# Performance work log

Hardware: AMD Instinct MI355X
Metric: run time of the kernel (lower is better)

Reference implementation:

```python
import jax, jax.numpy as jnp
import numpy as np

TAU = 2.0   # spikingjelly LIFNode default tau
VTH = 1.0   # config.vthreshold

@jax.custom_vjp
def atan_spike(x):
    # heaviside forward, ATan surrogate backward (spikingjelly surrogate.ATan, alpha=2)
    return (x >= 0).astype(x.dtype)

def _atan_fwd(x):
    return atan_spike(x), x

def _atan_bwd(x, g):
    alpha = 2.0
    return (g * (alpha / 2.0) / (1.0 + (jnp.pi / 2.0 * alpha * x) ** 2),)

atan_spike.defvjp(_atan_fwd, _atan_bwd)

def layer_norm(x, eps=1e-6):
    m = jnp.mean(x, axis=-1, keepdims=True)
    v = jnp.mean((x - m) ** 2, axis=-1, keepdims=True)
    return (x - m) * jax.lax.rsqrt(v + eps)

def time_shift(x):
    # ZeroPad2d((0,0,1,-1)): xx[:, t] = x[:, t-1], xx[:, 0] = 0
    return jnp.pad(x, ((0, 0), (1, 0), (0, 0)))[:, :-1]

def lif_multistep(x4):
    # spikingjelly LIFNode, step_mode='m', decay_input=True, hard reset to v_reset=0
    def step(v, xt):
        v = v + (xt - v) / TAU
        s = atan_spike(v - VTH)
        return v * (1.0 - s), s
    _, spikes = jax.lax.scan(step, jnp.zeros_like(x4[0]), x4)
    return spikes

def wkv(w, u, k, v):
    # RWKV-v4 numerically-stable WKV scan. w: [C] (negative), u: [C], k,v: [B,T,C]
    B, T, C = k.shape
    def step(carry, kv):
        aa, bb, pp = carry
        kt, vt = kv
        ww = u + kt
        p = jnp.maximum(pp, ww)
        e1 = jnp.exp(pp - p); e2 = jnp.exp(ww - p)
        y = (e1 * aa + e2 * vt) / (e1 * bb + e2)
        ww2 = pp + w
        p2 = jnp.maximum(ww2, kt)
        f1 = jnp.exp(ww2 - p2); f2 = jnp.exp(kt - p2)
        return (f1 * aa + f2 * vt, f1 * bb + f2, p2), y
    init = (jnp.zeros((B, C), k.dtype), jnp.zeros((B, C), k.dtype),
            jnp.full((B, C), -1e38, k.dtype))
    _, ys = jax.lax.scan(step, init, (jnp.moveaxis(k, 1, 0), jnp.moveaxis(v, 1, 0)))
    return jnp.moveaxis(ys, 0, 1)

def time_mix(h, time_decay, time_first, tmk, tmv, tmr, Wk, Wv, Wr, Wo):
    xx = time_shift(h)
    xk = h * tmk + xx * (1 - tmk)
    xv = h * tmv + xx * (1 - tmv)
    xr = h * tmr + xx * (1 - tmr)
    k = jnp.einsum('btc,oc->bto', xk, Wk)
    v = jnp.einsum('btc,oc->bto', xv, Wv)
    sr = jax.nn.sigmoid(jnp.einsum('btc,oc->bto', xr, Wr))
    y = wkv(-jnp.exp(time_decay), time_first, k, v)
    return jnp.einsum('btc,oc->bto', sr * y, Wo)

def channel_mix(h, cmk, cmr, Wck, Wcv, Wcr):
    xx = time_shift(h)
    xk = h * cmk + xx * (1 - cmk)
    xr = h * cmr + xx * (1 - cmr)
    k = jnp.square(jax.nn.relu(jnp.einsum('btc,hc->bth', xk, Wck)))
    kv = jnp.einsum('bth,ch->btc', k, Wcv)
    return jax.nn.sigmoid(jnp.einsum('btc,oc->bto', xr, Wcr)) * kv

def _forward(x, rt, time_decay, time_first, tmix_k, tmix_v, tmix_r,
             Wk, Wv, Wr, Wo, cmix_k, cmix_r, Wck, Wcv, Wcr,
             Wrm, brm, Wam, bam):
    B, P1, C = x.shape
    xc = jnp.concatenate([x, jnp.broadcast_to(rt, (B, P1, C))], axis=1)  # [B, 2*P1, C]
    att = time_mix(layer_norm(xc), time_decay, time_first,
                   tmix_k, tmix_v, tmix_r, Wk, Wv, Wr, Wo)
    att = lif_multistep(jnp.broadcast_to(att, (4,) + att.shape)).mean(0)
    xc = xc + att
    ffn = channel_mix(layer_norm(xc), cmix_k, cmix_r, Wck, Wcv, Wcr)
    ffn = lif_multistep(jnp.broadcast_to(ffn, (4,) + ffn.shape)).mean(0)
    xc = xc + ffn
    xo, rtok = xc[:, :P1], xc[:, P1:]
    r = jnp.einsum('bpc,qc->bpq', rtok, Wrm) + brm   # restruction_token_MLP [B,P1,P1]
    r = jnp.swapaxes(r, 1, 2)                        # permute(0,2,1)
    r = jnp.einsum('bpq,cq->bpc', r, Wam) + bam      # another_MLP [B,P1,C]
    return xo + xo * r

def setup_inputs() -> dict:
    key = jax.random.key(0)
    ks = jax.random.split(key, 20)
    B, P1, C = 8, 256, 1024
    H = 4 * C
    s = 0.02
    f32 = jnp.float32
    return {
        'x': jax.random.normal(ks[0], (B, P1, C), f32),
        'rt': jax.random.normal(ks[1], (1, P1, C), f32) * 0.5,
        'time_decay': jax.random.normal(ks[2], (C,), f32),
        'time_first': jax.random.normal(ks[3], (C,), f32) * 0.3,
        'tmix_k': jax.random.uniform(ks[4], (1, 1, C), f32),
        'tmix_v': jax.random.uniform(ks[5], (1, 1, C), f32),
        'tmix_r': jax.random.uniform(ks[6], (1, 1, C), f32),
        'Wk': jax.random.normal(ks[7], (C, C), f32) * s,
        'Wv': jax.random.normal(ks[8], (C, C), f32) * s,
        'Wr': jax.random.normal(ks[9], (C, C), f32) * s,
        'Wo': jax.random.normal(ks[10], (C, C), f32) * s,
        'cmix_k': jax.random.uniform(ks[11], (1, 1, C), f32),
        'cmix_r': jax.random.uniform(ks[12], (1, 1, C), f32),
        'Wck': jax.random.normal(ks[13], (H, C), f32) * s,
        'Wcv': jax.random.normal(ks[14], (C, H), f32) * s,
        'Wcr': jax.random.normal(ks[15], (C, C), f32) * s,
        'Wrm': jax.random.normal(ks[16], (P1, C), f32) * s,
        'brm': jax.random.normal(ks[17], (P1,), f32) * s,
        'Wam': jax.random.normal(ks[18], (C, P1), f32) * s,
        'bam': jax.random.normal(ks[19], (C,), f32) * s,
    }

def reference(x, rt, time_decay, time_first, tmix_k, tmix_v, tmix_r,
              Wk, Wv, Wr, Wo, cmix_k, cmix_r, Wck, Wcv, Wcr,
              Wrm, brm, Wam, bam):
    return _forward(x, rt, time_decay, time_first, tmix_k, tmix_v, tmix_r,
                    Wk, Wv, Wr, Wo, cmix_k, cmix_r, Wck, Wcv, Wcr,
                    Wrm, brm, Wam, bam)
```

## Files before the change

kernel.cpp:

```cpp
#include <hip/hip_runtime.h>
#include <hip/hip_bf16.h>
#include <math.h>
#include <stdint.h>

#define TB_ 8
#define TT_ 512
#define TC_ 1024
#define WKV_NCH 32
#define WKV_L 16

typedef __attribute__((ext_vector_type(8))) short bf16x8;
typedef __attribute__((ext_vector_type(4))) short s16x4;
typedef __attribute__((ext_vector_type(4))) float f32x4;

__device__ __forceinline__ float b2f(short u) {
  union { unsigned int i; float f; } x;
  x.i = ((unsigned int)(unsigned short)u) << 16;
  return x.f;
}
__device__ __forceinline__ short f2b(float f) {
  __hip_bfloat16 h = __float2bfloat16(f);
  return __builtin_bit_cast(short, h);
}
__device__ __forceinline__ float sigm(float x) { return 1.0f / (1.0f + expf(-x)); }

__device__ __forceinline__ float lif4(float a) {
  float v = 0.0f, acc = 0.0f;
#pragma unroll
  for (int i = 0; i < 4; ++i) {
    v += (a - v) * 0.5f;
    float s = (v >= 1.0f) ? 1.0f : 0.0f;
    acc += s;
    v *= (1.0f - s);
  }
  return acc * 0.25f;
}

__device__ __forceinline__ void gload16(const void* g, void* l) {
  __builtin_amdgcn_global_load_lds(
      (__attribute__((address_space(1))) void*)(g),
      (__attribute__((address_space(3))) void*)(l), 16, 0, 0);
}

template <int N>
__device__ __forceinline__ void waitv() {
  if constexpr (N == 0)  asm volatile("s_waitcnt vmcnt(0)" ::: "memory");
  else if constexpr (N == 2)  asm volatile("s_waitcnt vmcnt(2)" ::: "memory");
  else if constexpr (N == 3)  asm volatile("s_waitcnt vmcnt(3)" ::: "memory");
  else if constexpr (N == 4)  asm volatile("s_waitcnt vmcnt(4)" ::: "memory");
  else if constexpr (N == 6)  asm volatile("s_waitcnt vmcnt(6)" ::: "memory");
  else if constexpr (N == 8)  asm volatile("s_waitcnt vmcnt(8)" ::: "memory");
  else if constexpr (N == 9)  asm volatile("s_waitcnt vmcnt(9)" ::: "memory");
  else if constexpr (N == 12) asm volatile("s_waitcnt vmcnt(12)" ::: "memory");
  else static_assert(N == 0, "unsupported vmcnt");
}
__device__ __forceinline__ void barrier_() {
  asm volatile("s_barrier" ::: "memory");
}


__global__ __launch_bounds__(256) void build_xc(const float* __restrict__ x,
                                                const float* __restrict__ rt,
                                                float* __restrict__ xc) {
  int i = blockIdx.x * 256 + threadIdx.x;
  int c4 = i & 255;
  int t = (i >> 8) & 511;
  int b = i >> 17;
  float4 v;
  if (t < 256)
    v = ((const float4*)x)[(b * 256 + t) * 256 + c4];
  else
    v = ((const float4*)rt)[(t - 256) * 256 + c4];
  ((float4*)xc)[i] = v;
}

__global__ __launch_bounds__(256) void ln_rows_b(const float* __restrict__ src,
                                                 short* __restrict__ dst) {
  __shared__ float red[256];
  int64_t row = blockIdx.x;
  float4 v = ((const float4*)(src + row * TC_))[threadIdx.x];
  red[threadIdx.x] = v.x + v.y + v.z + v.w;
  __syncthreads();
  for (int off = 128; off > 0; off >>= 1) {
    if (threadIdx.x < off) red[threadIdx.x] += red[threadIdx.x + off];
    __syncthreads();
  }
  float mean = red[0] * (1.0f / 1024.0f);
  __syncthreads();
  float dx = v.x - mean, dy = v.y - mean, dz = v.z - mean, dw = v.w - mean;
  red[threadIdx.x] = dx * dx + dy * dy + dz * dz + dw * dw;
  __syncthreads();
  for (int off = 128; off > 0; off >>= 1) {
    if (threadIdx.x < off) red[threadIdx.x] += red[threadIdx.x + off];
    __syncthreads();
  }
  float rs = 1.0f / sqrtf(red[0] * (1.0f / 1024.0f) + 1e-6f);
  s16x4 o;
  o.x = f2b(dx * rs); o.y = f2b(dy * rs); o.z = f2b(dz * rs); o.w = f2b(dw * rs);
  *(s16x4*)(dst + row * TC_ + threadIdx.x * 4) = o;
}

__global__ __launch_bounds__(256) void mix3_b(const short* __restrict__ ln,
                                              const float* __restrict__ tk,
                                              const float* __restrict__ tv,
                                              const float* __restrict__ tr,
                                              short* __restrict__ xk,
                                              short* __restrict__ xv,
                                              short* __restrict__ xr) {
  int i = blockIdx.x * 256 + threadIdx.x;
  int c8 = i & 127;
  int t = (i >> 7) & 511;
  bf16x8 h = *(const bf16x8*)(ln + (int64_t)i * 8);
  bf16x8 s = {};
  if (t > 0) s = *(const bf16x8*)(ln + (int64_t)(i - 128) * 8);
  bf16x8 ok, ov, orr;
#pragma unroll
  for (int e = 0; e < 8; ++e) {
    float hf = b2f(h[e]), sf = b2f(s[e]);
    int c = c8 * 8 + e;
    float mk = tk[c], mv = tv[c], mr = tr[c];
    ok[e] = f2b(hf * mk + sf * (1.0f - mk));
    ov[e] = f2b(hf * mv + sf * (1.0f - mv));
    orr[e] = f2b(hf * mr + sf * (1.0f - mr));
  }
  *(bf16x8*)(xk + (int64_t)i * 8) = ok;
  *(bf16x8*)(xv + (int64_t)i * 8) = ov;
  *(bf16x8*)(xr + (int64_t)i * 8) = orr;
}

__global__ __launch_bounds__(256) void mix2_b(const short* __restrict__ ln,
                                              const float* __restrict__ tk,
                                              const float* __restrict__ tr,
                                              short* __restrict__ xk,
                                              short* __restrict__ xr) {
  int i = blockIdx.x * 256 + threadIdx.x;
  int c8 = i & 127;
  int t = (i >> 7) & 511;
  bf16x8 h = *(const bf16x8*)(ln + (int64_t)i * 8);
  bf16x8 s = {};
  if (t > 0) s = *(const bf16x8*)(ln + (int64_t)(i - 128) * 8);
  bf16x8 ok, orr;
#pragma unroll
  for (int e = 0; e < 8; ++e) {
    float hf = b2f(h[e]), sf = b2f(s[e]);
    int c = c8 * 8 + e;
    float mk = tk[c], mr = tr[c];
    ok[e] = f2b(hf * mk + sf * (1.0f - mk));
    orr[e] = f2b(hf * mr + sf * (1.0f - mr));
  }
  *(bf16x8*)(xk + (int64_t)i * 8) = ok;
  *(bf16x8*)(xr + (int64_t)i * 8) = orr;
}

__global__ __launch_bounds__(256) void cvt_b(const float* __restrict__ src,
                                             short* __restrict__ dst) {
  int64_t i = (int64_t)(blockIdx.x * 256 + threadIdx.x) * 8;
  float4 a = *(const float4*)(src + i);
  float4 b = *(const float4*)(src + i + 4);
  bf16x8 o;
  o[0] = f2b(a.x); o[1] = f2b(a.y); o[2] = f2b(a.z); o[3] = f2b(a.w);
  o[4] = f2b(b.x); o[5] = f2b(b.y); o[6] = f2b(b.z); o[7] = f2b(b.w);
  *(bf16x8*)(dst + i) = o;
}

__global__ __launch_bounds__(256) void cvt_rtok(const float* __restrict__ xc,
                                                short* __restrict__ dst) {
  int i = blockIdx.x * 256 + threadIdx.x;
  int b = i >> 15;
  int rem = i & 32767;
  const float* s = xc + (int64_t)b * 524288 + 262144 + (int64_t)rem * 8;
  float4 a = *(const float4*)s;
  float4 c = *(const float4*)(s + 4);
  bf16x8 o;
  o[0] = f2b(a.x); o[1] = f2b(a.y); o[2] = f2b(a.z); o[3] = f2b(a.w);
  o[4] = f2b(c.x); o[5] = f2b(c.y); o[6] = f2b(c.z); o[7] = f2b(c.w);
  *(bf16x8*)(dst + (int64_t)i * 8) = o;
}

__global__ __launch_bounds__(256) void wkv_p1(const float* __restrict__ td,
                                              const short* __restrict__ K,
                                              const short* __restrict__ V,
                                              float* __restrict__ Ca,
                                              float* __restrict__ Da,
                                              float* __restrict__ Qa) {
  int bx = blockIdx.x;
  int ch = bx >> 5;
  int b = (bx >> 2) & 7;
  int c = (bx & 3) * 256 + threadIdx.x;
  float w = -expf(td[c]);
  float aa = 0.0f, bb = 0.0f, pp = -1e38f;
  int64_t base = ((int64_t)b * TT_ + ch * WKV_L) * TC_ + c;
#pragma unroll
  for (int t = 0; t < WKV_L; ++t) {
    int64_t o = base + (int64_t)t * TC_;
    float kt = b2f(K[o]), vt = b2f(V[o]);
    float ww2 = pp + w;
    float p2 = fmaxf(ww2, kt);
    float e1 = expf(ww2 - p2);
    float e2 = expf(kt - p2);
    aa = e1 * aa + e2 * vt;
    bb = e1 * bb + e2;
    pp = p2;
  }
  int idx = ch * 8192 + b * 1024 + c;
  Ca[idx] = aa; Da[idx] = bb; Qa[idx] = pp;
}

__global__ __launch_bounds__(256) void wkv_p2(const float* __restrict__ td,
                                              const float* __restrict__ Ca,
                                              const float* __restrict__ Da,
                                              const float* __restrict__ Qa,
                                              float* __restrict__ Aa,
                                              float* __restrict__ Ba,
                                              float* __restrict__ Pa) {
  int i = blockIdx.x * 256 + threadIdx.x;
  int c = i & (TC_ - 1);
  float wL = -expf(td[c]) * (float)WKV_L;
  float aa = 0.0f, bb = 0.0f, pp = -1e38f;
#pragma unroll 4
  for (int ch = 0; ch < WKV_NCH; ++ch) {
    int idx = ch * 8192 + i;
    Aa[idx] = aa; Ba[idx] = bb; Pa[idx] = pp;
    float ppw = pp + wL;
    float q = Qa[idx];
    float p2 = fmaxf(ppw, q);
    float ea = expf(ppw - p2);
    float eb = expf(q - p2);
    aa = aa * ea + Ca[idx] * eb;
    bb = bb * ea + Da[idx] * eb;
    pp = p2;
  }
}

__global__ __launch_bounds__(256) void wkv_p3(const float* __restrict__ td,
                                              const float* __restrict__ tf,
                                              const short* __restrict__ K,
                                              const short* __restrict__ V,
                                              const short* __restrict__ SR,
                                              short* __restrict__ SRY,
                                              const float* __restrict__ Aa,
                                              const float* __restrict__ Ba,
                                              const float* __restrict__ Pa) {
  int bx = blockIdx.x;
  int ch = bx >> 5;
  int b = (bx >> 2) & 7;
  int c = (bx & 3) * 256 + threadIdx.x;
  float w = -expf(td[c]);
  float u = tf[c];
  int idx = ch * 8192 + b * 1024 + c;
  float aa = Aa[idx], bb = Ba[idx], pp = Pa[idx];
  int64_t base = ((int64_t)b * TT_ + ch * WKV_L) * TC_ + c;
#pragma unroll
  for (int t = 0; t < WKV_L; ++t) {
    int64_t o = base + (int64_t)t * TC_;
    float kt = b2f(K[o]), vt = b2f(V[o]);
    float ww = u + kt;
    float p = fmaxf(pp, ww);
    float E1 = expf(pp - p);
    float E2 = expf(ww - p);
    float y = (E1 * aa + E2 * vt) / (E1 * bb + E2);
    SRY[o] = f2b(y * b2f(SR[o]));
    float ww2 = pp + w;
    float p2 = fmaxf(ww2, kt);
    float e1 = expf(ww2 - p2);
    float e2 = expf(kt - p2);
    aa = e1 * aa + e2 * vt;
    bb = e1 * bb + e2;
    pp = p2;
  }
}

__global__ __launch_bounds__(64) void row_sum256(const float* __restrict__ Wam,
                                                 float* __restrict__ S) {
  int c = blockIdx.x;
  int lane = threadIdx.x;
  float4 v = ((const float4*)(Wam + (int64_t)c * 256))[lane];
  float s = v.x + v.y + v.z + v.w;
  for (int off = 32; off > 0; off >>= 1) s += __shfl_down(s, off);
  if (lane == 0) S[c] = s;
}

template <int BM, int BN, int EPI>
__global__ __launch_bounds__(256, 2) void gemm_bf16(
    const short* __restrict__ A, const short* __restrict__ B,
    void* __restrict__ Cp, int M, int N, int K,
    int64_t sA, int64_t sB, int64_t sC,
    const float* __restrict__ e0, const float* __restrict__ e1,
    const float* __restrict__ e2, const void* __restrict__ e3, int64_t sE) {
  constexpr int MF = BM / 32;
  constexpr int NF = BN / 32;
  constexpr int ASLOT = BM / 64;
  constexpr int BSLOT = BN / 64;
  constexpr int NL = ASLOT + BSLOT;
  constexpr int SBUF = (BM + BN) * 32;
  constexpr int D = 4;
  __shared__ short lds[D * SBUF];
  const int tid = threadIdx.x;

  const unsigned gx = gridDim.x, gy = gridDim.y;
  const unsigned nwg = gx * gy * gridDim.z;
  const unsigned lin = blockIdx.x + gx * (blockIdx.y + gy * blockIdx.z);
  const unsigned cs = nwg >> 3;
  const unsigned nl = (lin & 7) * cs + (lin >> 3);
  const unsigned bxs = nl % gx;
  const unsigned tmp = nl / gx;
  const unsigned bys = tmp % gy;
  const unsigned bz = tmp / gy;

  const int brow = bys * BM;
  const int bcol = bxs * BN;
  const short* Ab = A + bz * sA;
  const short* Bb = B + bz * sB;

  const int srow = ((tid >> 6) << 4) + (tid & 15);
  const int skc = ((tid >> 4) & 3) * 8;
  const short* gA[ASLOT];
  const short* gB[BSLOT];
#pragma unroll
  for (int s = 0; s < ASLOT; ++s)
    gA[s] = Ab + (int64_t)(brow + s * 64 + srow) * K + skc;
#pragma unroll
  for (int s = 0; s < BSLOT; ++s)
    gB[s] = Bb + (int64_t)(bcol + s * 64 + srow) * K + skc;

  const int lane = tid & 63, wid = tid >> 6;
  const int wr = wid >> 1, wc = wid & 1;

  f32x4 acc[MF][NF] = {};

  auto stage = [&](int buf, int k0) {
    short* d = lds + buf * SBUF;
#pragma unroll
    for (int s = 0; s < ASLOT; ++s)
      gload16(gA[s] + k0, d + s * 2048 + tid * 8);
#pragma unroll
    for (int s = 0; s < BSLOT; ++s)
      gload16(gB[s] + k0, d + BM * 32 + s * 2048 + tid * 8);
  };
  auto compute = [&](int buf) {
    const short* base = lds + buf * SBUF;
    bf16x8 af[MF], bfv[NF];
#pragma unroll
    for (int m = 0; m < MF; ++m)
      af[m] = *(const bf16x8*)(base + (wr * MF + m) * 512 + lane * 8);
#pragma unroll
    for (int n = 0; n < NF; ++n)
      bfv[n] = *(const bf16x8*)(base + BM * 32 + (wc * NF + n) * 512 + lane * 8);
#pragma unroll
    for (int m = 0; m < MF; ++m)
#pragma unroll
      for (int n = 0; n < NF; ++n)
        acc[m][n] = __builtin_amdgcn_mfma_f32_16x16x32_bf16(af[m], bfv[n],
                                                            acc[m][n], 0, 0, 0);
  };

  const int nst = K / 32;
#pragma unroll
  for (int d = 0; d < D - 1; ++d) stage(d, d * 32);
  for (int t = 0; t <= nst - D; ++t) {
    stage((t + D - 1) & (D - 1), (t + D - 1) * 32);
    waitv<(D - 1) * NL>();
    barrier_();
    compute(t & (D - 1));
    barrier_();
  }
  {
    int t = nst - D + 1;
    waitv<2 * NL>(); barrier_(); compute(t & (D - 1)); barrier_(); ++t;
    waitv<1 * NL>(); barrier_(); compute(t & (D - 1)); barrier_(); ++t;
    waitv<0>();      barrier_(); compute(t & (D - 1));
  }

  const int r0 = brow + wr * (BM / 2) + (lane >> 4) * 4;
  const int c0 = bcol + wc * (BN / 2) + (lane & 15);
#pragma unroll
  for (int m = 0; m < MF; ++m) {
#pragma unroll
    for (int j = 0; j < 4; ++j) {
      int row = r0 + m * 16 + j;
#pragma unroll
      for (int n = 0; n < NF; ++n) {
        int col = c0 + n * 16;
        float v = acc[m][n][j];
        int64_t idx = (int64_t)row * N + col;
        if (EPI == 0) {
          ((short*)Cp)[bz * sC + idx] = f2b(v);
        } else if (EPI == 1) {
          ((short*)Cp)[bz * sC + idx] = f2b(sigm(v));
        } else if (EPI == 2) {
          v = fmaxf(v, 0.0f);
          ((short*)Cp)[bz * sC + idx] = f2b(v * v);
        } else if (EPI == 3) {
          float r2 = v + e0[row] * e1[col] + e2[col];
          float xo = ((const float*)e3)[bz * sE + idx];
          ((float*)Cp)[bz * sC + idx] = xo * (1.0f + r2);
        } else if (EPI == 4) {
          float* XC = (float*)Cp;
          XC[idx] = XC[idx] + lif4(v);
        } else if (EPI == 5) {
          float* XC = (float*)Cp;
          float srr = b2f(((const short*)e3)[idx]);
          XC[idx] = XC[idx] + lif4(v * srr);
        } else if (EPI == 6) {
          ((short*)Cp)[bz * sC + idx] = f2b(bz == 2 ? sigm(v) : v);
        }
      }
    }
  }
}

extern "C" void kernel_launch(void* const* d_in, const int* in_sizes, int n_in,
                              void* d_out, int out_size, void* d_ws,
                              size_t ws_size, hipStream_t stream) {
  const float* x   = (const float*)d_in[0];
  const float* rt  = (const float*)d_in[1];
  const float* td  = (const float*)d_in[2];
  const float* tf  = (const float*)d_in[3];
  const float* tmk = (const float*)d_in[4];
  const float* tmv = (const float*)d_in[5];
  const float* tmr = (const float*)d_in[6];
  const float* Wk  = (const float*)d_in[7];
  const float* Wv  = (const float*)d_in[8];
  const float* Wr  = (const float*)d_in[9];
  const float* Wo  = (const float*)d_in[10];
  const float* cmk = (const float*)d_in[11];
  const float* cmr = (const float*)d_in[12];
  const float* Wck = (const float*)d_in[13];
  const float* Wcv = (const float*)d_in[14];
  const float* Wcr = (const float*)d_in[15];
  const float* Wrm = (const float*)d_in[16];
  const float* brm = (const float*)d_in[17];
  const float* Wam = (const float*)d_in[18];
  const float* bam = (const float*)d_in[19];
  float* out = (float*)d_out;

  const size_t MB = 1ull << 20;
  uint8_t* W8 = (uint8_t*)d_ws;
  float* XC   = (float*)(W8);
  short* L    = (short*)(W8 + 16 * MB);
  short* S1   = (short*)(W8 + 24 * MB);
  short* S2   = (short*)(W8 + 32 * MB);
  short* S3   = (short*)(W8 + 40 * MB);
  short* bWcv = (short*)(W8 + 48 * MB);
  short* bWk  = (short*)(W8 + 56 * MB);
  short* bWo  = (short*)(W8 + 62 * MB);
  short* bWcr = (short*)(W8 + 64 * MB);
  short* bWrm = (short*)(W8 + 66 * MB);
  short* bWam = (short*)(W8 + 66 * MB + 512 * 1024);
  short* KK   = (short*)(W8 + 67 * MB);
  short* VV   = (short*)(W8 + 75 * MB);
  short* RR   = (short*)(W8 + 83 * MB);
  float* Ca   = (float*)(W8 + 91 * MB);
  float* Da   = (float*)(W8 + 92 * MB);
  float* Qa   = (float*)(W8 + 93 * MB);
  float* Aa   = (float*)(W8 + 94 * MB);
  float* Ba   = (float*)(W8 + 95 * MB);
  float* Pa   = (float*)(W8 + 96 * MB);
  short* SRY  = S1;
  short* xk2  = S2;
  short* xr2  = S3;
  short* SRR  = S1;
  short* bWck = S3;
  short* H16  = KK;
  short* rtok = S2;
  short* Mt   = (short*)(W8 + 36 * MB);
  float* Sb   = (float*)(W8 + 24 * MB);

  dim3 blk(256);
  const int NV4 = 4096;
  const int NV8 = 2048;

  cvt_b<<<512, blk, 0, stream>>>(Wk, bWk);
  cvt_b<<<512, blk, 0, stream>>>(Wv, bWk + 1048576);
  cvt_b<<<512, blk, 0, stream>>>(Wr, bWk + 2097152);
  cvt_b<<<512, blk, 0, stream>>>(Wo, bWo);
  cvt_b<<<512, blk, 0, stream>>>(Wcr, bWcr);
  cvt_b<<<128, blk, 0, stream>>>(Wrm, bWrm);
  cvt_b<<<128, blk, 0, stream>>>(Wam, bWam);

  build_xc<<<NV4, blk, 0, stream>>>(x, rt, XC);
  ln_rows_b<<<TB_ * TT_, blk, 0, stream>>>(XC, L);
  mix3_b<<<NV8, blk, 0, stream>>>(L, tmk, tmv, tmr, S1, S2, S3);

  gemm_bf16<128, 128, 6><<<dim3(8, 32, 3), blk, 0, stream>>>(
      S1, bWk, KK, 4096, 1024, 1024, 4194304, 1048576, 4194304,
      nullptr, nullptr, nullptr, nullptr, 0);
  wkv_p1<<<WKV_NCH * TB_ * 4, blk, 0, stream>>>(td, KK, VV, Ca, Da, Qa);
  wkv_p2<<<32, blk, 0, stream>>>(td, Ca, Da, Qa, Aa, Ba, Pa);
  wkv_p3<<<WKV_NCH * TB_ * 4, blk, 0, stream>>>(td, tf, KK, VV, RR, SRY,
                                                Aa, Ba, Pa);
  gemm_bf16<128, 128, 4><<<dim3(8, 32, 1), blk, 0, stream>>>(
      SRY, bWo, XC, 4096, 1024, 1024, 0, 0, 0,
      nullptr, nullptr, nullptr, nullptr, 0);
  ln_rows_b<<<TB_ * TT_, blk, 0, stream>>>(XC, L);
  mix2_b<<<NV8, blk, 0, stream>>>(L, cmk, cmr, xk2, xr2);
  gemm_bf16<128, 128, 1><<<dim3(8, 32, 1), blk, 0, stream>>>(
      xr2, bWcr, SRR, 4096, 1024, 1024, 0, 0, 0,
      nullptr, nullptr, nullptr, nullptr, 0);
  cvt_b<<<2048, blk, 0, stream>>>(Wck, bWck);
  cvt_b<<<2048, blk, 0, stream>>>(Wcv, bWcv);
  gemm_bf16<128, 128, 2><<<dim3(32, 32, 1), blk, 0, stream>>>(
      xk2, bWck, H16, 4096, 4096, 1024, 0, 0, 0,
      nullptr, nullptr, nullptr, nullptr, 0);
  gemm_bf16<128, 128, 5><<<dim3(8, 32, 1), blk, 0, stream>>>(
      H16, bWcv, XC, 4096, 1024, 4096, 0, 0, 0,
      nullptr, nullptr, nullptr, SRR, 0);
  cvt_rtok<<<1024, blk, 0, stream>>>(XC, rtok);
  gemm_bf16<64, 64, 0><<<dim3(4, 4, 8), blk, 0, stream>>>(
      bWrm, rtok, Mt, 256, 256, 1024, 0, (int64_t)256 * 1024,
      (int64_t)256 * 256, nullptr, nullptr, nullptr, nullptr, 0);
  row_sum256<<<1024, dim3(64), 0, stream>>>(Wam, Sb);
  gemm_bf16<64, 64, 3><<<dim3(16, 4, 8), blk, 0, stream>>>(
      Mt, bWam, out, 256, 1024, 256, (int64_t)256 * 256, 0,
      (int64_t)256 * 1024, brm, Sb, bam, XC, (int64_t)512 * 1024);
}
```

Before: 355.8 us.

## Tune GEMM pipeline depth and occupancy per call; fuse input gather with LayerNorm

The GEMM kernel now takes its LDS pipeline depth and minimum-waves launch bound as template parameters, with matching vmcnt waits and tail handling for depths 2, 4 and 8. Each call site picks its own setting: deep 8-stage pipelines at one wave-group per CU for the K-heavy or small-grid GEMMs, and shallow 2-stage pipelines with higher occupancy for the others. Separately, the copy kernel that concatenated x and rt is fused into the first LayerNorm, so the assembled rows are read once and written alongside the normalized output. The risks are larger LDS use (128KB at depth 8) lowering occupancy, and less latency hiding at depth 2.

```diff
diff --git a/kernel.cpp b/kernel.cpp
--- a/kernel.cpp
+++ b/kernel.cpp
@@ -46,12 +46,14 @@
 __device__ __forceinline__ void waitv() {
   if constexpr (N == 0)  asm volatile("s_waitcnt vmcnt(0)" ::: "memory");
   else if constexpr (N == 2)  asm volatile("s_waitcnt vmcnt(2)" ::: "memory");
-  else if constexpr (N == 3)  asm volatile("s_waitcnt vmcnt(3)" ::: "memory");
   else if constexpr (N == 4)  asm volatile("s_waitcnt vmcnt(4)" ::: "memory");
   else if constexpr (N == 6)  asm volatile("s_waitcnt vmcnt(6)" ::: "memory");
   else if constexpr (N == 8)  asm volatile("s_waitcnt vmcnt(8)" ::: "memory");
-  else if constexpr (N == 9)  asm volatile("s_waitcnt vmcnt(9)" ::: "memory");
   else if constexpr (N == 12) asm volatile("s_waitcnt vmcnt(12)" ::: "memory");
+  else if constexpr (N == 16) asm volatile("s_waitcnt vmcnt(16)" ::: "memory");
+  else if constexpr (N == 20) asm volatile("s_waitcnt vmcnt(20)" ::: "memory");
+  else if constexpr (N == 24) asm volatile("s_waitcnt vmcnt(24)" ::: "memory");
+  else if constexpr (N == 28) asm volatile("s_waitcnt vmcnt(28)" ::: "memory");
   else static_assert(N == 0, "unsupported vmcnt");
 }
 __device__ __forceinline__ void barrier_() {
@@ -59,19 +61,36 @@
 }
 
 
-__global__ __launch_bounds__(256) void build_xc(const float* __restrict__ x,
+__global__ __launch_bounds__(256) void ln_first(const float* __restrict__ x,
                                                 const float* __restrict__ rt,
-                                                float* __restrict__ xc) {
-  int i = blockIdx.x * 256 + threadIdx.x;
-  int c4 = i & 255;
-  int t = (i >> 8) & 511;
-  int b = i >> 17;
-  float4 v;
-  if (t < 256)
-    v = ((const float4*)x)[(b * 256 + t) * 256 + c4];
-  else
-    v = ((const float4*)rt)[(t - 256) * 256 + c4];
-  ((float4*)xc)[i] = v;
+                                                float* __restrict__ xc,
+                                                short* __restrict__ dst) {
+  __shared__ float red[256];
+  int row = blockIdx.x;
+  int t = row & 511, b = row >> 9;
+  const float* src = (t < 256) ? x + (int64_t)(b * 256 + t) * TC_
+                               : rt + (int64_t)(t - 256) * TC_;
+  float4 v = ((const float4*)src)[threadIdx.x];
+  ((float4*)(xc + (int64_t)row * TC_))[threadIdx.x] = v;
+  red[threadIdx.x] = v.x + v.y + v.z + v.w;
+  __syncthreads();
+  for (int off = 128; off > 0; off >>= 1) {
+    if (threadIdx.x < off) red[threadIdx.x] += red[threadIdx.x + off];
+    __syncthreads();
+  }
+  float mean = red[0] * (1.0f / 1024.0f);
+  __syncthreads();
+  float dx = v.x - mean, dy = v.y - mean, dz = v.z - mean, dw = v.w - mean;
+  red[threadIdx.x] = dx * dx + dy * dy + dz * dz + dw * dw;
+  __syncthreads();
+  for (int off = 128; off > 0; off >>= 1) {
+    if (threadIdx.x < off) red[threadIdx.x] += red[threadIdx.x + off];
+    __syncthreads();
+  }
+  float rs = 1.0f / sqrtf(red[0] * (1.0f / 1024.0f) + 1e-6f);
+  s16x4 o;
+  o.x = f2b(dx * rs); o.y = f2b(dy * rs); o.z = f2b(dz * rs); o.w = f2b(dw * rs);
+  *(s16x4*)(dst + (int64_t)row * TC_ + threadIdx.x * 4) = o;
 }
 
 __global__ __launch_bounds__(256) void ln_rows_b(const float* __restrict__ src,
@@ -280,8 +299,8 @@
   if (lane == 0) S[c] = s;
 }
 
-template <int BM, int BN, int EPI>
-__global__ __launch_bounds__(256, 2) void gemm_bf16(
+template <int BM, int BN, int EPI, int D, int MINW>
+__global__ __launch_bounds__(256, MINW) void gemm_bf16(
     const short* __restrict__ A, const short* __restrict__ B,
     void* __restrict__ Cp, int M, int N, int K,
     int64_t sA, int64_t sB, int64_t sC,
@@ -293,7 +312,6 @@
   constexpr int BSLOT = BN / 64;
   constexpr int NL = ASLOT + BSLOT;
   constexpr int SBUF = (BM + BN) * 32;
-  constexpr int D = 4;
   __shared__ short lds[D * SBUF];
   const int tid = threadIdx.x;
 
@@ -366,9 +384,17 @@
   }
   {
     int t = nst - D + 1;
-    waitv<2 * NL>(); barrier_(); compute(t & (D - 1)); barrier_(); ++t;
-    waitv<1 * NL>(); barrier_(); compute(t & (D - 1)); barrier_(); ++t;
-    waitv<0>();      barrier_(); compute(t & (D - 1));
+    if constexpr (D >= 8) {
+      waitv<6 * NL>(); barrier_(); compute(t & (D - 1)); barrier_(); ++t;
+      waitv<5 * NL>(); barrier_(); compute(t & (D - 1)); barrier_(); ++t;
+      waitv<4 * NL>(); barrier_(); compute(t & (D - 1)); barrier_(); ++t;
+      waitv<3 * NL>(); barrier_(); compute(t & (D - 1)); barrier_(); ++t;
+    }
+    if constexpr (D >= 4) {
+      waitv<2 * NL>(); barrier_(); compute(t & (D - 1)); barrier_(); ++t;
+      waitv<1 * NL>(); barrier_(); compute(t & (D - 1)); barrier_(); ++t;
+    }
+    waitv<0>(); barrier_(); compute(t & (D - 1));
   }
 
   const int r0 = brow + wr * (BM / 2) + (lane >> 4) * 4;
@@ -467,7 +493,6 @@
   float* Sb   = (float*)(W8 + 24 * MB);
 
   dim3 blk(256);
-  const int NV4 = 4096;
   const int NV8 = 2048;
 
   cvt_b<<<512, blk, 0, stream>>>(Wk, bWk);
@@ -478,39 +503,38 @@
   cvt_b<<<128, blk, 0, stream>>>(Wrm, bWrm);
   cvt_b<<<128, blk, 0, stream>>>(Wam, bWam);
 
-  build_xc<<<NV4, blk, 0, stream>>>(x, rt, XC);
-  ln_rows_b<<<TB_ * TT_, blk, 0, stream>>>(XC, L);
+  ln_first<<<TB_ * TT_, blk, 0, stream>>>(x, rt, XC, L);
   mix3_b<<<NV8, blk, 0, stream>>>(L, tmk, tmv, tmr, S1, S2, S3);
 
-  gemm_bf16<128, 128, 6><<<dim3(8, 32, 3), blk, 0, stream>>>(
+  gemm_bf16<128, 128, 6, 2, 3><<<dim3(8, 32, 3), blk, 0, stream>>>(
       S1, bWk, KK, 4096, 1024, 1024, 4194304, 1048576, 4194304,
       nullptr, nullptr, nullptr, nullptr, 0);
   wkv_p1<<<WKV_NCH * TB_ * 4, blk, 0, stream>>>(td, KK, VV, Ca, Da, Qa);
   wkv_p2<<<32, blk, 0, stream>>>(td, Ca, Da, Qa, Aa, Ba, Pa);
   wkv_p3<<<WKV_NCH * TB_ * 4, blk, 0, stream>>>(td, tf, KK, VV, RR, SRY,
                                                 Aa, Ba, Pa);
-  gemm_bf16<128, 128, 4><<<dim3(8, 32, 1), blk, 0, stream>>>(
+  gemm_bf16<128, 128, 4, 8, 1><<<dim3(8, 32, 1), blk, 0, stream>>>(
       SRY, bWo, XC, 4096, 1024, 1024, 0, 0, 0,
       nullptr, nullptr, nullptr, nullptr, 0);
   ln_rows_b<<<TB_ * TT_, blk, 0, stream>>>(XC, L);
   mix2_b<<<NV8, blk, 0, stream>>>(L, cmk, cmr, xk2, xr2);
-  gemm_bf16<128, 128, 1><<<dim3(8, 32, 1), blk, 0, stream>>>(
+  gemm_bf16<128, 128, 1, 8, 1><<<dim3(8, 32, 1), blk, 0, stream>>>(
       xr2, bWcr, SRR, 4096, 1024, 1024, 0, 0, 0,
       nullptr, nullptr, nullptr, nullptr, 0);
   cvt_b<<<2048, blk, 0, stream>>>(Wck, bWck);
   cvt_b<<<2048, blk, 0, stream>>>(Wcv, bWcv);
-  gemm_bf16<128, 128, 2><<<dim3(32, 32, 1), blk, 0, stream>>>(
+  gemm_bf16<128, 128, 2, 2, 4><<<dim3(32, 32, 1), blk, 0, stream>>>(
       xk2, bWck, H16, 4096, 4096, 1024, 0, 0, 0,
       nullptr, nullptr, nullptr, nullptr, 0);
-  gemm_bf16<128, 128, 5><<<dim3(8, 32, 1), blk, 0, stream>>>(
+  gemm_bf16<128, 128, 5, 8, 1><<<dim3(8, 32, 1), blk, 0, stream>>>(
       H16, bWcv, XC, 4096, 1024, 4096, 0, 0, 0,
       nullptr, nullptr, nullptr, SRR, 0);
   cvt_rtok<<<1024, blk, 0, stream>>>(XC, rtok);
-  gemm_bf16<64, 64, 0><<<dim3(4, 4, 8), blk, 0, stream>>>(
+  gemm_bf16<64, 64, 0, 2, 2><<<dim3(4, 4, 8), blk, 0, stream>>>(
       bWrm, rtok, Mt, 256, 256, 1024, 0, (int64_t)256 * 1024,
       (int64_t)256 * 256, nullptr, nullptr, nullptr, nullptr, 0);
   row_sum256<<<1024, dim3(64), 0, stream>>>(Wam, Sb);
-  gemm_bf16<64, 64, 3><<<dim3(16, 4, 8), blk, 0, stream>>>(
+  gemm_bf16<64, 64, 3, 2, 2><<<dim3(16, 4, 8), blk, 0, stream>>>(
       Mt, bWam, out, 256, 1024, 256, (int64_t)256 * 256, 0,
       (int64_t)256 * 1024, brm, Sb, bam, XC, (int64_t)512 * 1024);
 }
```

Result: no change. 355.3 us (-0.2%).
